# Optimization experiments

Hardware: AMD Instinct MI355X
Metric: run time of the kernel (lower is better)

The kernel has to match this reference:

```python
import jax, jax.numpy as jnp
import numpy as np
import math


def l2norm(x, axis):
    n = jnp.linalg.norm(x, axis=axis, keepdims=True)
    return x / jnp.maximum(n, 1e-12)


def token_pooling(x, w1, b1, w2, b2, p, w3, b3, w4, b4, eps=1e-6):
    # x: [B, L, dim_in]
    h = jnp.maximum(x @ w1 + b1, 0.0) @ w2 + b2        # [B, L, 512]
    h = l2norm(h, -1)
    # GeM over token dim L (avg_pool1d over full length == mean)
    g = jnp.mean(jnp.clip(h, eps, None) ** p, axis=1) ** (1.0 / p)  # [B, 512]
    o = jnp.maximum(g @ w3 + b3, 0.0) @ w4 + b4        # [B, dim_out]
    return l2norm(o, -1)


def sinkhorn_log(S_aug, log_a, log_b, num_iters=3):
    # S_aug: [B, m+1, n]; reg = 1.0
    M = S_aug
    u = jnp.zeros_like(log_a)
    v = jnp.zeros_like(log_b)
    def body(carry, _):
        u, v = carry
        u = log_a - jax.nn.logsumexp(M + v[:, None, :], axis=2)
        v = log_b - jax.nn.logsumexp(M + u[:, :, None], axis=1)
        return (u, v), None
    (u, v), _ = jax.lax.scan(body, (u, v), None, length=num_iters)
    return M + u[:, :, None] + v[:, None, :]


def setup_inputs() -> dict:
    key = jax.random.key(0)
    ks = jax.random.split(key, 16)
    B, S, N, C = 4, 4, 1029, 2048
    def w(k, shape):
        return jax.random.normal(k, shape, dtype=jnp.float32) * 0.02
    inp = {
        "tokens": jax.random.normal(ks[0], (B, S, N, C), dtype=jnp.float32),
        "patch_start_idx": 5,
        # camera token pooling
        "cam_w1": w(ks[1], (2048, 1024)), "cam_b1": jnp.zeros((1024,), jnp.float32),
        "cam_w2": w(ks[2], (1024, 512)),  "cam_b2": jnp.zeros((512,), jnp.float32),
        "cam_p":  jnp.ones((1,), jnp.float32) * 3.0,
        "cam_w3": w(ks[3], (512, 512)),   "cam_b3": jnp.zeros((512,), jnp.float32),
        "cam_w4": w(ks[4], (512, 256)),   "cam_b4": jnp.zeros((256,), jnp.float32),
        # register token pooling
        "reg_w1": w(ks[5], (2048, 1024)), "reg_b1": jnp.zeros((1024,), jnp.float32),
        "reg_w2": w(ks[6], (1024, 512)),  "reg_b2": jnp.zeros((512,), jnp.float32),
        "reg_p":  jnp.ones((1,), jnp.float32) * 3.0,
        "reg_w3": w(ks[7], (512, 512)),   "reg_b3": jnp.zeros((512,), jnp.float32),
        "reg_w4": w(ks[8], (512, 256)),   "reg_b4": jnp.zeros((256,), jnp.float32),
        # patch cluster features (1x1 convs == linear over channel dim)
        "pf_w1": w(ks[9], (2048, 512)),   "pf_b1": jnp.zeros((512,), jnp.float32),
        "pf_w2": w(ks[10], (512, 128)),   "pf_b2": jnp.zeros((128,), jnp.float32),
        # patch scores
        "ps_w1": w(ks[11], (2048, 512)),  "ps_b1": jnp.zeros((512,), jnp.float32),
        "ps_w2": w(ks[12], (512, 64)),    "ps_b2": jnp.zeros((64,), jnp.float32),
        "dust_bin": jnp.array(1.0, jnp.float32),
    }
    return inp


def reference(tokens, patch_start_idx, cam_w1, cam_b1, cam_w2, cam_b2, cam_p, cam_w3, cam_b3, cam_w4, cam_b4, reg_w1, reg_b1, reg_w2, reg_b2, reg_p, reg_w3, reg_b3, reg_w4, reg_b4, pf_w1, pf_b1, pf_w2, pf_b2, ps_w1, ps_b1, ps_w2, ps_b2, dust_bin):
    B, S, N, C = tokens.shape
    psi = int(patch_start_idx)
    # camera token: [B, S, C]
    camera = token_pooling(tokens[:, :, 0], cam_w1, cam_b1, cam_w2, cam_b2, cam_p, cam_w3, cam_b3, cam_w4, cam_b4)
    # register tokens: [B, S*(psi-1), C]
    reg_tok = tokens[:, :, 1:psi].reshape(B, S * (psi - 1), C)
    register = token_pooling(reg_tok, reg_w1, reg_b1, reg_w2, reg_b2, reg_p, reg_w3, reg_b3, reg_w4, reg_b4)
    # patch tokens flattened over (S, Np): n = S*Np
    patch = tokens[:, :, psi:].reshape(B, -1, C)              # [B, n, C]
    n = patch.shape[1]
    feats = jnp.maximum(patch @ pf_w1 + pf_b1, 0.0) @ pf_w2 + pf_b2   # [B, n, 128]
    scores = jnp.maximum(patch @ ps_w1 + ps_b1, 0.0) @ ps_w2 + ps_b2  # [B, n, 64]
    S_mat = jnp.swapaxes(scores, 1, 2)                        # [B, m, n]
    m = S_mat.shape[1]
    # augment with dustbin row
    dust_row = jnp.broadcast_to(dust_bin, (B, 1, n)).astype(S_mat.dtype)
    S_aug = jnp.concatenate([S_mat, dust_row], axis=1)        # [B, m+1, n]
    norm = -math.log(n + m)
    log_a = jnp.full((m + 1,), norm, dtype=S_mat.dtype).at[-1].add(math.log(n - m))
    log_b = jnp.full((n,), norm, dtype=S_mat.dtype)
    log_a = jnp.broadcast_to(log_a, (B, m + 1))
    log_b = jnp.broadcast_to(log_b, (B, n))
    log_P = sinkhorn_log(S_aug, log_a, log_b, num_iters=3) - norm
    p = jnp.exp(log_P)[:, :-1, :]                             # [B, m, n]
    # (f * p).sum(-1) as batched matmul: [B, cluster_dim, m]
    pooled = jnp.einsum('bnc,bkn->bck', feats, p)
    patch_result = l2norm(pooled, 1).reshape(B, -1)           # [B, cluster_dim*m]
    return jnp.concatenate([patch_result, camera, register], axis=-1)
```

## Files before the change

kernel.cpp:

```cpp
#include <hip/hip_runtime.h>

typedef unsigned short u16;
typedef unsigned int u32;

#define B_ 4
#define S_ 4
#define NTOK 1029
#define CDIM 2048
#define PSI 5
#define NPB 4096
#define MROWS 16384
#define N1 1024
#define N2 256
#define MD 64
#define MA 65

using bf16x8 = __attribute__((ext_vector_type(8))) short;
using f32x4  = __attribute__((ext_vector_type(4))) float;
using u16x8  = __attribute__((ext_vector_type(8))) unsigned short;

typedef __attribute__((address_space(1))) const void global_cvoid;
typedef __attribute__((address_space(3))) void lds_void;

__device__ __forceinline__ u16 f2b(float f) {
  u32 u = __builtin_bit_cast(u32, f);
  u32 r = (u + 0x7fffu + ((u >> 16) & 1u)) >> 16;
  return (u16)r;
}

__global__ void k_prep_patch(const float* __restrict__ tokens, u16* __restrict__ Abf,
                             const float* __restrict__ pfw1, const float* __restrict__ psw1,
                             const float* __restrict__ pfw2, const float* __restrict__ psw2,
                             const float* __restrict__ pfb1, const float* __restrict__ psb1,
                             const float* __restrict__ pfb2, const float* __restrict__ psb2,
                             u16* __restrict__ W1t, u16* __restrict__ W2t,
                             float* __restrict__ b1c, float* __restrict__ b2c) {
  __shared__ float tile[32][33];
  int id = blockIdx.x, tid = threadIdx.x;
  if (id < 16384) {
    size_t idx = (size_t)id * 256 + tid;
    size_t r = idx >> 8;
    int cv = (int)(idx & 255) << 3;
    int b = (int)(r >> 12), s = (int)((r >> 10) & 3), j = (int)(r & 1023);
    const float* src = tokens + ((size_t)((b * S_ + s) * NTOK + PSI + j)) * CDIM + cv;
    float4 v0 = *(const float4*)src;
    float4 v1 = *(const float4*)(src + 4);
    u16x8 o;
    o[0] = f2b(v0.x); o[1] = f2b(v0.y); o[2] = f2b(v0.z); o[3] = f2b(v0.w);
    o[4] = f2b(v1.x); o[5] = f2b(v1.y); o[6] = f2b(v1.z); o[7] = f2b(v1.w);
    *(u16x8*)(Abf + r * CDIM + cv) = o;
    return;
  }
  int id2 = id - 16384;
  int tx = tid & 31, ty = tid >> 5;
  if (id2 < 2048) {
    int kb = (id2 & 63) * 32, nb = (id2 >> 6) * 32;
    #pragma unroll
    for (int i = 0; i < 4; ++i) {
      int k = kb + ty + i * 8, n = nb + tx;
      tile[ty + i * 8][tx] = (n < 512) ? pfw1[(size_t)k * 512 + n] : psw1[(size_t)k * 512 + (n - 512)];
    }
    __syncthreads();
    #pragma unroll
    for (int i = 0; i < 4; ++i) {
      int n = nb + ty + i * 8, k = kb + tx;
      W1t[(size_t)n * CDIM + k] = f2b(tile[tx][ty + i * 8]);
    }
  } else if (id2 < 2304) {
    int i2 = id2 - 2048;
    int kb = (i2 & 31) * 32, jb = (i2 >> 5) * 32;
    #pragma unroll
    for (int i = 0; i < 4; ++i) {
      int k = kb + ty + i * 8, j = jb + tx;
      float v = 0.f;
      if (j < 128) { if (k < 512) v = pfw2[(size_t)k * 128 + j]; }
      else if (j < 192) { if (k >= 512) v = psw2[(size_t)(k - 512) * 64 + (j - 128)]; }
      tile[ty + i * 8][tx] = v;
    }
    __syncthreads();
    #pragma unroll
    for (int i = 0; i < 4; ++i) {
      int j = jb + ty + i * 8, k = kb + tx;
      W2t[(size_t)j * N1 + k] = f2b(tile[tx][ty + i * 8]);
    }
  } else {
    int t = (id2 - 2304) * 256 + tid;
    if (t < 1024) b1c[t] = (t < 512) ? pfb1[t] : psb1[t - 512];
    if (t < 256)  b2c[t] = (t < 128) ? pfb2[t] : ((t < 192) ? psb2[t - 128] : 0.f);
  }
}

__global__ void k_pack_cr(const float* __restrict__ camw1, const float* __restrict__ regw1,
                          const float* __restrict__ camw2, const float* __restrict__ regw2,
                          const float* __restrict__ tokens,
                          u16* __restrict__ Bt1cr, u16* __restrict__ Bt2cr,
                          u16* __restrict__ Acr) {
  __shared__ float tile[32][33];
  int id = blockIdx.x, tid = threadIdx.x;
  int tx = tid & 31, ty = tid >> 5;
  if (id < 4096) {
    const float* src = (id < 2048) ? camw1 : regw1;
    u16* dst = Bt1cr + ((id < 2048) ? 0 : (size_t)1024 * CDIM);
    int i2 = id & 2047;
    int kb = (i2 & 63) * 32, nb = (i2 >> 6) * 32;
    #pragma unroll
    for (int i = 0; i < 4; ++i)
      tile[ty + i * 8][tx] = src[(size_t)(kb + ty + i * 8) * 1024 + nb + tx];
    __syncthreads();
    #pragma unroll
    for (int i = 0; i < 4; ++i)
      dst[(size_t)(nb + ty + i * 8) * CDIM + kb + tx] = f2b(tile[tx][ty + i * 8]);
  } else if (id < 5120) {
    int i3 = id - 4096;
    const float* src = (i3 < 512) ? camw2 : regw2;
    u16* dst = Bt2cr + ((i3 < 512) ? 0 : (size_t)512 * N1);
    int i2 = i3 & 511;
    int kb = (i2 & 31) * 32, nb = (i2 >> 5) * 32;
    #pragma unroll
    for (int i = 0; i < 4; ++i)
      tile[ty + i * 8][tx] = src[(size_t)(kb + ty + i * 8) * 512 + nb + tx];
    __syncthreads();
    #pragma unroll
    for (int i = 0; i < 4; ++i)
      dst[(size_t)(nb + ty + i * 8) * N1 + kb + tx] = f2b(tile[tx][ty + i * 8]);
  } else {
    int r = id - 5120;
    int c0 = tid << 3;
    u16x8 o;
    if (r >= 80) {
      #pragma unroll
      for (int i = 0; i < 8; ++i) o[i] = 0;
    } else {
      const float* src;
      if (r < 16) { int b = r >> 2, s = r & 3; src = tokens + ((size_t)(b * S_ + s) * NTOK) * CDIM; }
      else { int r2 = r - 16; int b = r2 >> 4, q = r2 & 15, s = q >> 2, t = (q & 3) + 1;
             src = tokens + ((size_t)(b * S_ + s) * NTOK + t) * CDIM; }
      float4 v0 = *(const float4*)(src + c0);
      float4 v1 = *(const float4*)(src + c0 + 4);
      o[0] = f2b(v0.x); o[1] = f2b(v0.y); o[2] = f2b(v0.z); o[3] = f2b(v0.w);
      o[4] = f2b(v1.x); o[5] = f2b(v1.y); o[6] = f2b(v1.z); o[7] = f2b(v1.w);
    }
    *(u16x8*)(Acr + (size_t)r * CDIM + c0) = o;
  }
}

#define STAGE_TILE(buf, k0)                                                    \
  {                                                                            \
    _Pragma("unroll")                                                          \
    for (int r = 0; r < 4; ++r) {                                              \
      __builtin_amdgcn_global_load_lds(                                        \
          (global_cvoid*)(A + abase + (size_t)(r * 32) * K + (k0)),            \
          (lds_void*)(&As[buf][lofs + r * 2048]), 16, 0, 0);                   \
      __builtin_amdgcn_global_load_lds(                                        \
          (global_cvoid*)(Bt + bbase + (size_t)(r * 32) * K + (k0)),           \
          (lds_void*)(&Bs[buf][lofs + r * 2048]), 16, 0, 0);                   \
    }                                                                          \
  }

#define COMPUTE_TILE(buf)                                                      \
  {                                                                            \
    _Pragma("unroll")                                                          \
    for (int kk = 0; kk < 64; kk += 32) {                                      \
      const int csw = (kk + hi8) ^ ((lane & 7) << 3);                          \
      bf16x8 af[4], bfr[4];                                                    \
      _Pragma("unroll")                                                        \
      for (int i = 0; i < 4; ++i) {                                            \
        af[i]  = *(const bf16x8*)&As[buf][((wr << 6) + (i << 4) + (lane & 15)) * 64 + csw]; \
        bfr[i] = *(const bf16x8*)&Bs[buf][((wc << 6) + (i << 4) + (lane & 15)) * 64 + csw]; \
      }                                                                        \
      _Pragma("unroll")                                                        \
      for (int mi = 0; mi < 4; ++mi)                                           \
        _Pragma("unroll")                                                      \
        for (int ni = 0; ni < 4; ++ni)                                         \
          acc[mi][ni] = __builtin_amdgcn_mfma_f32_16x16x32_bf16(af[mi], bfr[ni], acc[mi][ni], 0, 0, 0); \
    }                                                                          \
  }

template <int RELU, int OUTBF, int WRSC>
__global__ __launch_bounds__(256, 2)
void k_gemm(const u16* __restrict__ A, const u16* __restrict__ Bt,
            const float* __restrict__ bias, void* __restrict__ Cout,
            int M, int N, int K, float* __restrict__ ScOut) {
  __shared__ u16 As[2][128 * 64];
  __shared__ u16 Bs[2][128 * 64];
  const int tid = threadIdx.x;
  const int lane = tid & 63;
  const int wave = tid >> 6;
  const int tM = blockIdx.x << 7;
  const int tN = blockIdx.y << 7;
  const int wr = wave >> 1, wc = wave & 1;
  const int hi8 = (lane >> 4) << 3;

  const int srow = (wave << 3) + (lane >> 3);
  const int scolsw = ((lane & 7) ^ (lane >> 3)) << 3;
  const size_t abase = (size_t)(tM + srow) * K + scolsw;
  const size_t bbase = (size_t)(tN + srow) * K + scolsw;
  const int lofs = (wave << 9) + (lane << 3);

  f32x4 acc[4][4];
  #pragma unroll
  for (int i = 0; i < 4; ++i)
    #pragma unroll
    for (int j = 0; j < 4; ++j)
      acc[i][j] = (f32x4){0.f, 0.f, 0.f, 0.f};

  const int nt = K >> 6;
  STAGE_TILE(0, 0)
  STAGE_TILE(1, 64)
  for (int t = 0; t < nt; t += 2) {
    asm volatile("s_waitcnt vmcnt(8)" ::: "memory");
    __builtin_amdgcn_s_barrier();
    COMPUTE_TILE(0)
    __builtin_amdgcn_s_barrier();
    if (t + 2 < nt) STAGE_TILE(0, (t + 2) << 6)
    if (t + 1 == nt - 1) {
      asm volatile("s_waitcnt vmcnt(0)" ::: "memory");
    } else {
      asm volatile("s_waitcnt vmcnt(8)" ::: "memory");
    }
    __builtin_amdgcn_s_barrier();
    COMPUTE_TILE(1)
    __builtin_amdgcn_s_barrier();
    if (t + 3 < nt) STAGE_TILE(1, (t + 3) << 6)
  }

  #pragma unroll
  for (int ni = 0; ni < 4; ++ni) {
    const int col = tN + (wc << 6) + (ni << 4) + (lane & 15);
    const float bv = bias[col];
    #pragma unroll
    for (int mi = 0; mi < 4; ++mi) {
      #pragma unroll
      for (int j = 0; j < 4; ++j) {
        const int row = tM + (wr << 6) + (mi << 4) + ((lane >> 4) << 2) + j;
        float vv = acc[mi][ni][j] + bv;
        if (RELU) vv = fmaxf(vv, 0.f);
        if (OUTBF) ((u16*)Cout)[(size_t)row * N + col] = f2b(vv);
        else       ((float*)Cout)[(size_t)row * N + col] = vv;
        if (WRSC) {
          if (col >= 128 && col < 192)
            ScOut[((size_t)((row >> 12) * MD + (col - 128))) * NPB + (row & 4095)] = vv;
        }
      }
    }
  }
}

__global__ __launch_bounds__(256, 2)
void k_gemm_splitk(const u16* __restrict__ A, const u16* __restrict__ Bt,
                   float* __restrict__ part, int N, int K, int KC) {
  __shared__ u16 As1[128 * 64];
  __shared__ u16 Bs1[128 * 64];
  const int tid = threadIdx.x;
  const int lane = tid & 63;
  const int wave = tid >> 6;
  const int tN = blockIdx.y << 7;
  const int kb = blockIdx.z * KC;
  const int wr = wave >> 1, wc = wave & 1;
  const int srow = (wave << 3) + (lane >> 3);
  const int scol = (lane & 7) << 3;
  const size_t abase = (size_t)srow * K + scol;
  const size_t bbase = (size_t)(tN + srow) * K + scol;
  u16* asw = &As1[(wave << 9) + (lane << 3)];
  u16* bsw = &Bs1[(wave << 9) + (lane << 3)];

  f32x4 acc[4][4];
  #pragma unroll
  for (int i = 0; i < 4; ++i)
    #pragma unroll
    for (int j = 0; j < 4; ++j)
      acc[i][j] = (f32x4){0.f, 0.f, 0.f, 0.f};

  for (int k0 = kb; k0 < kb + KC; k0 += 64) {
    #pragma unroll
    for (int r = 0; r < 4; ++r) {
      __builtin_amdgcn_global_load_lds(
          (global_cvoid*)(A + abase + (size_t)(r * 32) * K + k0),
          (lds_void*)(asw + r * 2048), 16, 0, 0);
      __builtin_amdgcn_global_load_lds(
          (global_cvoid*)(Bt + bbase + (size_t)(r * 32) * K + k0),
          (lds_void*)(bsw + r * 2048), 16, 0, 0);
    }
    __syncthreads();
    #pragma unroll
    for (int kk = 0; kk < 64; kk += 32) {
      bf16x8 af[4], bfr[4];
      #pragma unroll
      for (int i = 0; i < 4; ++i) {
        af[i]  = *(const bf16x8*)&As1[((wr << 6) + (i << 4) + (lane & 15)) * 64 + kk + ((lane >> 4) << 3)];
        bfr[i] = *(const bf16x8*)&Bs1[((wc << 6) + (i << 4) + (lane & 15)) * 64 + kk + ((lane >> 4) << 3)];
      }
      #pragma unroll
      for (int mi = 0; mi < 4; ++mi)
        #pragma unroll
        for (int ni = 0; ni < 4; ++ni)
          acc[mi][ni] = __builtin_amdgcn_mfma_f32_16x16x32_bf16(af[mi], bfr[ni], acc[mi][ni], 0, 0, 0);
    }
    __syncthreads();
  }

  float* dst = part + (size_t)blockIdx.z * 128 * N;
  #pragma unroll
  for (int ni = 0; ni < 4; ++ni) {
    const int col = tN + (wc << 6) + (ni << 4) + (lane & 15);
    #pragma unroll
    for (int mi = 0; mi < 4; ++mi) {
      #pragma unroll
      for (int j = 0; j < 4; ++j) {
        const int row = (wr << 6) + (mi << 4) + ((lane >> 4) << 2) + j;
        dst[(size_t)row * N + col] = acc[mi][ni][j];
      }
    }
  }
}

__global__ void k_cr_fin1(const float* __restrict__ part1,
                          const float* __restrict__ camb1, const float* __restrict__ regb1,
                          u16* __restrict__ A2) {
  int r = blockIdx.x;
  int j = blockIdx.y * 256 + threadIdx.x;
  if (r >= 80) { A2[(size_t)r * N1 + j] = 0; return; }
  bool cam = (r < 16);
  int cm = j + (cam ? 0 : 1024);
  float s = 0.f;
  #pragma unroll
  for (int kc = 0; kc < 8; ++kc) s += part1[((size_t)kc * 128 + r) * 2048 + cm];
  s += cam ? camb1[j] : regb1[j];
  A2[(size_t)r * N1 + j] = f2b(fmaxf(s, 0.f));
}

__global__ __launch_bounds__(512)
void k_cr_fin2(const float* __restrict__ part2,
               const float* __restrict__ camb2, const float* __restrict__ regb2,
               const float* __restrict__ camp, const float* __restrict__ regp,
               float* __restrict__ hp) {
  __shared__ float red[8];
  int r = blockIdx.x;
  int j = threadIdx.x;
  bool cam = (r < 16);
  int cm = j + (cam ? 0 : 512);
  float s = 0.f;
  #pragma unroll
  for (int kc = 0; kc < 8; ++kc) s += part2[((size_t)kc * 128 + r) * 1024 + cm];
  s += cam ? camb2[j] : regb2[j];
  float ss = s * s;
  #pragma unroll
  for (int o = 32; o; o >>= 1) ss += __shfl_down(ss, o);
  if ((j & 63) == 0) red[j >> 6] = ss;
  __syncthreads();
  float tot = 0.f;
  #pragma unroll
  for (int i = 0; i < 8; ++i) tot += red[i];
  float inv = 1.f / fmaxf(sqrtf(tot), 1e-12f);
  float t = fmaxf(s * inv, 1e-6f);
  hp[(size_t)r * 512 + j] = powf(t, cam ? camp[0] : regp[0]);
}

__global__ __launch_bounds__(512)
void k_cr3a(const float* __restrict__ hp, const float* __restrict__ camp,
            const float* __restrict__ regp, float* __restrict__ gsb) {
  int pb = blockIdx.x;
  bool cam = (pb < 4);
  int b = pb & 3;
  float p = cam ? camp[0] : regp[0];
  int L = cam ? 4 : 16;
  int row0 = cam ? b * 4 : 16 + b * 16;
  int o = threadIdx.x;
  float s = 0.f;
  for (int r = 0; r < L; ++r) s += hp[(size_t)(row0 + r) * 512 + o];
  gsb[pb * 512 + o] = powf(s / (float)L, 1.f / p);
}

__global__ __launch_bounds__(512)
void k_cr3b(const float* __restrict__ gsb,
            const float* __restrict__ camw3, const float* __restrict__ regw3,
            const float* __restrict__ camb3, const float* __restrict__ regb3,
            float* __restrict__ o1b) {
  __shared__ float gls[512];
  __shared__ float part[4][128];
  int pb = blockIdx.x, och = blockIdx.y;
  bool cam = (pb < 4);
  const float* W3 = cam ? camw3 : regw3;
  const float* B3 = cam ? camb3 : regb3;
  int tid = threadIdx.x;
  gls[tid] = gsb[pb * 512 + tid];
  __syncthreads();
  int col = tid & 127, kq = tid >> 7;
  int o = (och << 7) + col;
  float acc = 0.f;
  const float* w = W3 + (size_t)(kq << 7) * 512 + o;
  #pragma unroll 8
  for (int kk = 0; kk < 128; ++kk) acc += gls[(kq << 7) + kk] * w[(size_t)kk * 512];
  part[kq][col] = acc;
  __syncthreads();
  if (kq == 0) {
    float s = part[0][col] + part[1][col] + part[2][col] + part[3][col] + B3[o];
    o1b[pb * 512 + o] = fmaxf(s, 0.f);
  }
}

__global__ __launch_bounds__(512)
void k_cr3c(const float* __restrict__ o1b,
            const float* __restrict__ camw4, const float* __restrict__ regw4,
            const float* __restrict__ camb4, const float* __restrict__ regb4,
            float* __restrict__ out) {
  __shared__ float o1s[512];
  __shared__ float part[2][256];
  __shared__ float vsq[256];
  __shared__ float red[4];
  int pb = blockIdx.x;
  bool cam = (pb < 4);
  int path = pb >> 2, b = pb & 3;
  const float* W4 = cam ? camw4 : regw4;
  const float* B4 = cam ? camb4 : regb4;
  int tid = threadIdx.x;
  o1s[tid] = o1b[pb * 512 + tid];
  __syncthreads();
  int col = tid & 255, kh = tid >> 8;
  float acc = 0.f;
  const float* w = W4 + (size_t)(kh << 8) * 256 + col;
  #pragma unroll 8
  for (int kk = 0; kk < 256; ++kk) acc += o1s[(kh << 8) + kk] * w[(size_t)kk * 256];
  part[kh][col] = acc;
  __syncthreads();
  float val = 0.f;
  if (kh == 0) {
    val = part[0][col] + part[1][col] + B4[col];
    vsq[col] = val * val;
  }
  __syncthreads();
  float ss = (tid < 256) ? vsq[tid] : 0.f;
  #pragma unroll
  for (int o = 32; o; o >>= 1) ss += __shfl_down(ss, o);
  if (tid < 256 && (tid & 63) == 0) red[tid >> 6] = ss;
  __syncthreads();
  if (kh == 0) {
    float tot = red[0] + red[1] + red[2] + red[3];
    float inv = 1.f / fmaxf(sqrtf(tot), 1e-12f);
    out[(size_t)b * 8704 + 8192 + path * 256 + col] = val * inv;
  }
}

__global__ void k_sink_u(const float* __restrict__ Sc, const float* __restrict__ v,
                         float* __restrict__ u, const float* __restrict__ dust) {
  __shared__ float redm[4], reds[4];
  int b = blockIdx.x / MA, k = blockIdx.x % MA;
  const float* vb = v + (size_t)b * NPB;
  int tid = threadIdx.x;
  float mx = -1e30f, s = 0.f;
  if (k < MD) {
    const float* row = Sc + ((size_t)(b * MD) + k) * NPB;
    for (int n = tid; n < NPB; n += 256) {
      float x = row[n] + vb[n];
      float m2 = fmaxf(mx, x);
      s = s * __expf(mx - m2) + __expf(x - m2);
      mx = m2;
    }
  } else {
    float d0 = dust[0];
    for (int n = tid; n < NPB; n += 256) {
      float x = d0 + vb[n];
      float m2 = fmaxf(mx, x);
      s = s * __expf(mx - m2) + __expf(x - m2);
      mx = m2;
    }
  }
  #pragma unroll
  for (int o = 32; o; o >>= 1) {
    float mo = __shfl_down(mx, o), so = __shfl_down(s, o);
    float m2 = fmaxf(mx, mo);
    s = s * __expf(mx - m2) + so * __expf(mo - m2);
    mx = m2;
  }
  if ((tid & 63) == 0) { redm[tid >> 6] = mx; reds[tid >> 6] = s; }
  __syncthreads();
  if (tid == 0) {
    float M = redm[0];
    #pragma unroll
    for (int i = 1; i < 4; ++i) M = fmaxf(M, redm[i]);
    float S = 0.f;
    #pragma unroll
    for (int i = 0; i < 4; ++i) S += reds[i] * __expf(redm[i] - M);
    const float nrm = -logf((float)(NPB + MD));
    float la = (k == MD) ? (nrm + logf((float)(NPB - MD))) : nrm;
    u[b * MA + k] = la - (M + __logf(S));
  }
}

__global__ void k_sink_v(const float* __restrict__ Sc, const float* __restrict__ u,
                         float* __restrict__ v, const float* __restrict__ dust) {
  __shared__ float us[MA];
  int b = blockIdx.x >> 4;
  int n = ((blockIdx.x & 15) << 8) + threadIdx.x;
  if (threadIdx.x < MA) us[threadIdx.x] = u[b * MA + threadIdx.x];
  __syncthreads();
  const float* Sb = Sc + (size_t)b * MD * NPB + n;
  float d0 = dust[0];
  float mx = d0 + us[MD];
  for (int k = 0; k < MD; ++k) mx = fmaxf(mx, Sb[(size_t)k * NPB] + us[k]);
  float s = __expf(d0 + us[MD] - mx);
  for (int k = 0; k < MD; ++k) s += __expf(Sb[(size_t)k * NPB] + us[k] - mx);
  const float nrm = -logf((float)(NPB + MD));
  v[(size_t)b * NPB + n] = nrm - (mx + __logf(s));
}

__global__ __launch_bounds__(256)
void k_pooled1(const float* __restrict__ FS, const float* __restrict__ Sc,
               const float* __restrict__ u, const float* __restrict__ v,
               float* __restrict__ partial) {
  __shared__ float Fs[64][132];
  __shared__ float Ps[64][68];
  int b = blockIdx.x >> 6, j = blockIdx.x & 63;
  int n0 = j << 6;
  int tid = threadIdx.x;
  {
    int r = tid >> 5;
    int c4 = (tid & 31) << 2;
    #pragma unroll
    for (int i = 0; i < 8; ++i) {
      int n = r + (i << 3);
      float4 vv = *(const float4*)&FS[((size_t)(b * NPB + n0 + n)) * N2 + c4];
      *(float4*)&Fs[n][c4] = vv;
    }
  }
  {
    const float nrm = -logf((float)(NPB + MD));
    int r = tid >> 4;
    int c4 = (tid & 15) << 2;
    #pragma unroll
    for (int i = 0; i < 4; ++i) {
      int k = r + (i << 4);
      float uk = u[b * MA + k];
      float4 sv = *(const float4*)&Sc[((size_t)(b * MD) + k) * NPB + n0 + c4];
      float4 vv = *(const float4*)&v[(size_t)b * NPB + n0 + c4];
      float4 o;
      o.x = __expf(sv.x + uk + vv.x - nrm);
      o.y = __expf(sv.y + uk + vv.y - nrm);
      o.z = __expf(sv.z + uk + vv.z - nrm);
      o.w = __expf(sv.w + uk + vv.w - nrm);
      *(float4*)&Ps[k][c4] = o;
    }
  }
  __syncthreads();
  int tc = tid & 31, tk = tid >> 5;
  int c0 = tc << 2, k0 = tk << 3;
  float acc[4][8];
  #pragma unroll
  for (int i = 0; i < 4; ++i)
    #pragma unroll
    for (int kk = 0; kk < 8; ++kk) acc[i][kk] = 0.f;
  for (int n = 0; n < 64; ++n) {
    float4 f = *(const float4*)&Fs[n][c0];
    float pv[8];
    #pragma unroll
    for (int kk = 0; kk < 8; ++kk) pv[kk] = Ps[k0 + kk][n];
    #pragma unroll
    for (int i = 0; i < 4; ++i) {
      float fv = ((const float*)&f)[i];
      #pragma unroll
      for (int kk = 0; kk < 8; ++kk) acc[i][kk] += fv * pv[kk];
    }
  }
  float* dst = partial + ((size_t)(b * 64 + j) << 13);
  #pragma unroll
  for (int i = 0; i < 4; ++i) {
    float4 lo = {acc[i][0], acc[i][1], acc[i][2], acc[i][3]};
    float4 hi = {acc[i][4], acc[i][5], acc[i][6], acc[i][7]};
    *(float4*)&dst[((c0 + i) << 6) + k0] = lo;
    *(float4*)&dst[((c0 + i) << 6) + k0 + 4] = hi;
  }
}

__global__ void k_pooled2(const float* __restrict__ partial, float* __restrict__ pooled) {
  int o = blockIdx.x * 256 + threadIdx.x;
  int b = o >> 13, rem = o & 8191;
  const float* src = partial + ((size_t)b << 19) + rem;
  float s = 0.f;
  #pragma unroll 8
  for (int j = 0; j < 64; ++j) s += src[(size_t)j << 13];
  pooled[o] = s;
}

__global__ void k_patch_out(const float* __restrict__ pooled, float* __restrict__ out) {
  int b = blockIdx.x >> 6, k = blockIdx.x & 63;
  int tid = threadIdx.x;
  float v0 = pooled[((size_t)(b * 128) + tid) * MD + k];
  float v1 = pooled[((size_t)(b * 128) + 64 + tid) * MD + k];
  float ss = v0 * v0 + v1 * v1;
  #pragma unroll
  for (int o = 32; o; o >>= 1) ss += __shfl_down(ss, o);
  ss = __shfl(ss, 0);
  float inv = 1.f / fmaxf(sqrtf(ss), 1e-12f);
  out[(size_t)b * 8704 + tid * 64 + k] = v0 * inv;
  out[(size_t)b * 8704 + (64 + tid) * 64 + k] = v1 * inv;
}

#define OFF_ABF 0u
#define OFF_SC 0u
#define OFF_U 4259840u
#define OFF_V 4263936u
#define OFF_POOL 8523776u
#define OFF_HP 8982528u
#define OFF_H 67108864u
#define OFF_PART OFF_H
#define OFF_CP1 75497472u
#define OFF_GSB OFF_CP1
#define OFF_O1B 75513856u
#define OFF_CP2 83886080u
#define OFF_BT1CR 88080384u
#define OFF_BT2CR 96468992u
#define OFF_ACR 98566144u
#define OFF_A2 99090432u
#define OFF_FS 100663296u
#define OFF_W1T 117440512u
#define OFF_W2T 121634816u
#define OFF_B1C 122159104u
#define OFF_B2C 122163200u

extern "C" void kernel_launch(void* const* d_in, const int* in_sizes, int n_in,
                              void* d_out, int out_size, void* d_ws, size_t ws_size,
                              hipStream_t stream) {
  (void)in_sizes; (void)n_in; (void)out_size; (void)ws_size;
  const float* tokens = (const float*)d_in[0];
  const float* cam_w1 = (const float*)d_in[2];
  const float* cam_b1 = (const float*)d_in[3];
  const float* cam_w2 = (const float*)d_in[4];
  const float* cam_b2 = (const float*)d_in[5];
  const float* cam_p  = (const float*)d_in[6];
  const float* cam_w3 = (const float*)d_in[7];
  const float* cam_b3 = (const float*)d_in[8];
  const float* cam_w4 = (const float*)d_in[9];
  const float* cam_b4 = (const float*)d_in[10];
  const float* reg_w1 = (const float*)d_in[11];
  const float* reg_b1 = (const float*)d_in[12];
  const float* reg_w2 = (const float*)d_in[13];
  const float* reg_b2 = (const float*)d_in[14];
  const float* reg_p  = (const float*)d_in[15];
  const float* reg_w3 = (const float*)d_in[16];
  const float* reg_b3 = (const float*)d_in[17];
  const float* reg_w4 = (const float*)d_in[18];
  const float* reg_b4 = (const float*)d_in[19];
  const float* pf_w1  = (const float*)d_in[20];
  const float* pf_b1  = (const float*)d_in[21];
  const float* pf_w2  = (const float*)d_in[22];
  const float* pf_b2  = (const float*)d_in[23];
  const float* ps_w1  = (const float*)d_in[24];
  const float* ps_b1  = (const float*)d_in[25];
  const float* ps_w2  = (const float*)d_in[26];
  const float* ps_b2  = (const float*)d_in[27];
  const float* dust   = (const float*)d_in[28];
  float* out = (float*)d_out;
  char* ws = (char*)d_ws;

  u16* Abf = (u16*)(ws + OFF_ABF);
  float* Sc = (float*)(ws + OFF_SC);
  float* ub = (float*)(ws + OFF_U);
  float* vb = (float*)(ws + OFF_V);
  float* pooled = (float*)(ws + OFF_POOL);
  float* hp = (float*)(ws + OFF_HP);
  u16* H   = (u16*)(ws + OFF_H);
  float* partial = (float*)(ws + OFF_PART);
  float* cp1 = (float*)(ws + OFF_CP1);
  float* gsb = (float*)(ws + OFF_GSB);
  float* o1b = (float*)(ws + OFF_O1B);
  float* cp2 = (float*)(ws + OFF_CP2);
  u16* Bt1cr = (u16*)(ws + OFF_BT1CR);
  u16* Bt2cr = (u16*)(ws + OFF_BT2CR);
  u16* Acr = (u16*)(ws + OFF_ACR);
  u16* A2  = (u16*)(ws + OFF_A2);
  float* FS = (float*)(ws + OFF_FS);
  u16* W1t = (u16*)(ws + OFF_W1T);
  u16* W2t = (u16*)(ws + OFF_W2T);
  float* b1c = (float*)(ws + OFF_B1C);
  float* b2c = (float*)(ws + OFF_B2C);

  hipMemsetAsync(vb, 0, (size_t)B_ * NPB * sizeof(float), stream);

  k_prep_patch<<<18692, 256, 0, stream>>>(tokens, Abf, pf_w1, ps_w1, pf_w2, ps_w2,
                                          pf_b1, ps_b1, pf_b2, ps_b2,
                                          W1t, W2t, b1c, b2c);
  k_gemm<1, 1, 0><<<dim3(128, 8), 256, 0, stream>>>(Abf, W1t, b1c, (void*)H,
                                                    MROWS, N1, CDIM, nullptr);
  k_gemm<0, 0, 1><<<dim3(128, 2), 256, 0, stream>>>(H, W2t, b2c, (void*)FS,
                                                    MROWS, N2, N1, Sc);

  k_pack_cr<<<5248, 256, 0, stream>>>(cam_w1, reg_w1, cam_w2, reg_w2, tokens,
                                      Bt1cr, Bt2cr, Acr);
  k_gemm_splitk<<<dim3(1, 16, 8), 256, 0, stream>>>(Acr, Bt1cr, cp1, 2048, CDIM, 256);
  k_cr_fin1<<<dim3(128, 4), 256, 0, stream>>>(cp1, cam_b1, reg_b1, A2);
  k_gemm_splitk<<<dim3(1, 8, 8), 256, 0, stream>>>(A2, Bt2cr, cp2, 1024, N1, 128);
  k_cr_fin2<<<80, 512, 0, stream>>>(cp2, cam_b2, reg_b2, cam_p, reg_p, hp);
  k_cr3a<<<8, 512, 0, stream>>>(hp, cam_p, reg_p, gsb);
  k_cr3b<<<dim3(8, 4), 512, 0, stream>>>(gsb, cam_w3, reg_w3, cam_b3, reg_b3, o1b);
  k_cr3c<<<8, 512, 0, stream>>>(o1b, cam_w4, reg_w4, cam_b4, reg_b4, out);

  for (int it = 0; it < 3; ++it) {
    k_sink_u<<<B_ * MA, 256, 0, stream>>>(Sc, vb, ub, dust);
    k_sink_v<<<B_ * 16, 256, 0, stream>>>(Sc, ub, vb, dust);
  }
  k_pooled1<<<B_ * 64, 256, 0, stream>>>(FS, Sc, ub, vb, partial);
  k_pooled2<<<128, 256, 0, stream>>>(partial, pooled);
  k_patch_out<<<B_ * MD, 64, 0, stream>>>(pooled, out);
}
```

Before: 243.1 us.

## Fuse camera/register head kernels and restructure Sinkhorn column update

Merges the three small pooling-head kernels (GeM mean, first MLP layer, second MLP layer with L2 norm) into one kernel per batch/path, so two launches and the global round-trips through scratch buffers are gone. The fused kernel uses 8 blocks, so the first MLP layer, which was previously spread over 32 blocks, now runs over output chunks serially inside each block. Separately, the Sinkhorn v-update now uses 256 blocks of 64 threads instead of 64 blocks of 256, stages the score tile in shared memory, and computes the logsumexp with an online single pass instead of two passes.

```diff
diff --git a/kernel.cpp b/kernel.cpp
--- a/kernel.cpp
+++ b/kernel.cpp
@@ -357,75 +357,67 @@
 }
 
 __global__ __launch_bounds__(512)
-void k_cr3a(const float* __restrict__ hp, const float* __restrict__ camp,
-            const float* __restrict__ regp, float* __restrict__ gsb) {
-  int pb = blockIdx.x;
-  bool cam = (pb < 4);
-  int b = pb & 3;
-  float p = cam ? camp[0] : regp[0];
-  int L = cam ? 4 : 16;
-  int row0 = cam ? b * 4 : 16 + b * 16;
-  int o = threadIdx.x;
-  float s = 0.f;
-  for (int r = 0; r < L; ++r) s += hp[(size_t)(row0 + r) * 512 + o];
-  gsb[pb * 512 + o] = powf(s / (float)L, 1.f / p);
-}
-
-__global__ __launch_bounds__(512)
-void k_cr3b(const float* __restrict__ gsb,
-            const float* __restrict__ camw3, const float* __restrict__ regw3,
-            const float* __restrict__ camb3, const float* __restrict__ regb3,
-            float* __restrict__ o1b) {
+void k_cr3f(const float* __restrict__ hp,
+            const float* __restrict__ camp, const float* __restrict__ camw3,
+            const float* __restrict__ camb3, const float* __restrict__ camw4,
+            const float* __restrict__ camb4,
+            const float* __restrict__ regp, const float* __restrict__ regw3,
+            const float* __restrict__ regb3, const float* __restrict__ regw4,
+            const float* __restrict__ regb4,
+            float* __restrict__ out) {
   __shared__ float gls[512];
-  __shared__ float part[4][128];
-  int pb = blockIdx.x, och = blockIdx.y;
-  bool cam = (pb < 4);
-  const float* W3 = cam ? camw3 : regw3;
-  const float* B3 = cam ? camb3 : regb3;
-  int tid = threadIdx.x;
-  gls[tid] = gsb[pb * 512 + tid];
-  __syncthreads();
-  int col = tid & 127, kq = tid >> 7;
-  int o = (och << 7) + col;
-  float acc = 0.f;
-  const float* w = W3 + (size_t)(kq << 7) * 512 + o;
-  #pragma unroll 8
-  for (int kk = 0; kk < 128; ++kk) acc += gls[(kq << 7) + kk] * w[(size_t)kk * 512];
-  part[kq][col] = acc;
-  __syncthreads();
-  if (kq == 0) {
-    float s = part[0][col] + part[1][col] + part[2][col] + part[3][col] + B3[o];
-    o1b[pb * 512 + o] = fmaxf(s, 0.f);
-  }
-}
-
-__global__ __launch_bounds__(512)
-void k_cr3c(const float* __restrict__ o1b,
-            const float* __restrict__ camw4, const float* __restrict__ regw4,
-            const float* __restrict__ camb4, const float* __restrict__ regb4,
-            float* __restrict__ out) {
   __shared__ float o1s[512];
-  __shared__ float part[2][256];
+  __shared__ float partb[4][128];
+  __shared__ float partc[2][256];
   __shared__ float vsq[256];
   __shared__ float red[4];
   int pb = blockIdx.x;
   bool cam = (pb < 4);
   int path = pb >> 2, b = pb & 3;
+  const float* W3 = cam ? camw3 : regw3;
+  const float* B3 = cam ? camb3 : regb3;
   const float* W4 = cam ? camw4 : regw4;
   const float* B4 = cam ? camb4 : regb4;
+  float p = cam ? camp[0] : regp[0];
+  int L = cam ? 4 : 16;
+  int row0 = cam ? b * 4 : 16 + b * 16;
   int tid = threadIdx.x;
-  o1s[tid] = o1b[pb * 512 + tid];
+
+  {
+    float s = 0.f;
+    for (int r = 0; r < L; ++r) s += hp[(size_t)(row0 + r) * 512 + tid];
+    gls[tid] = powf(s / (float)L, 1.f / p);
+  }
   __syncthreads();
+
+  {
+    int col = tid & 127, kq = tid >> 7;
+    for (int och = 0; och < 4; ++och) {
+      int oc = (och << 7) + col;
+      float acc = 0.f;
+      const float* w = W3 + (size_t)(kq << 7) * 512 + oc;
+      #pragma unroll 8
+      for (int kk = 0; kk < 128; ++kk) acc += gls[(kq << 7) + kk] * w[(size_t)kk * 512];
+      partb[kq][col] = acc;
+      __syncthreads();
+      if (kq == 0)
+        o1s[oc] = fmaxf(partb[0][col] + partb[1][col] + partb[2][col] + partb[3][col] + B3[oc], 0.f);
+      __syncthreads();
+    }
+  }
+
   int col = tid & 255, kh = tid >> 8;
   float acc = 0.f;
-  const float* w = W4 + (size_t)(kh << 8) * 256 + col;
-  #pragma unroll 8
-  for (int kk = 0; kk < 256; ++kk) acc += o1s[(kh << 8) + kk] * w[(size_t)kk * 256];
-  part[kh][col] = acc;
+  {
+    const float* w = W4 + (size_t)(kh << 8) * 256 + col;
+    #pragma unroll 8
+    for (int kk = 0; kk < 256; ++kk) acc += o1s[(kh << 8) + kk] * w[(size_t)kk * 256];
+    partc[kh][col] = acc;
+  }
   __syncthreads();
   float val = 0.f;
   if (kh == 0) {
-    val = part[0][col] + part[1][col] + B4[col];
+    val = partc[0][col] + partc[1][col] + B4[col];
     vsq[col] = val * val;
   }
   __syncthreads();
@@ -487,21 +479,31 @@
   }
 }
 
-__global__ void k_sink_v(const float* __restrict__ Sc, const float* __restrict__ u,
-                         float* __restrict__ v, const float* __restrict__ dust) {
+__global__ __launch_bounds__(64)
+void k_sink_v(const float* __restrict__ Sc, const float* __restrict__ u,
+              float* __restrict__ v, const float* __restrict__ dust) {
+  __shared__ float tile[64][65];
   __shared__ float us[MA];
-  int b = blockIdx.x >> 4;
-  int n = ((blockIdx.x & 15) << 8) + threadIdx.x;
-  if (threadIdx.x < MA) us[threadIdx.x] = u[b * MA + threadIdx.x];
+  int b = blockIdx.x >> 6;
+  int n0 = (blockIdx.x & 63) << 6;
+  int tid = threadIdx.x;
+  us[tid] = u[b * MA + tid];
+  if (tid == 0) us[MD] = u[b * MA + MD];
+  const float* Sb = Sc + (size_t)b * MD * NPB + n0;
+  #pragma unroll 8
+  for (int k = 0; k < MD; ++k)
+    tile[k][tid] = Sb[(size_t)k * NPB + tid];
   __syncthreads();
-  const float* Sb = Sc + (size_t)b * MD * NPB + n;
-  float d0 = dust[0];
-  float mx = d0 + us[MD];
-  for (int k = 0; k < MD; ++k) mx = fmaxf(mx, Sb[(size_t)k * NPB] + us[k]);
-  float s = __expf(d0 + us[MD] - mx);
-  for (int k = 0; k < MD; ++k) s += __expf(Sb[(size_t)k * NPB] + us[k] - mx);
+  float mx = dust[0] + us[MD], s = 1.f;
+  #pragma unroll 8
+  for (int k = 0; k < MD; ++k) {
+    float x = tile[k][tid] + us[k];
+    float m2 = fmaxf(mx, x);
+    s = s * __expf(mx - m2) + __expf(x - m2);
+    mx = m2;
+  }
   const float nrm = -logf((float)(NPB + MD));
-  v[(size_t)b * NPB + n] = nrm - (mx + __logf(s));
+  v[(size_t)b * NPB + n0 + tid] = nrm - (mx + __logf(s));
 }
 
 __global__ __launch_bounds__(256)
@@ -604,8 +606,6 @@
 #define OFF_H 67108864u
 #define OFF_PART OFF_H
 #define OFF_CP1 75497472u
-#define OFF_GSB OFF_CP1
-#define OFF_O1B 75513856u
 #define OFF_CP2 83886080u
 #define OFF_BT1CR 88080384u
 #define OFF_BT2CR 96468992u
@@ -661,8 +661,6 @@
   u16* H   = (u16*)(ws + OFF_H);
   float* partial = (float*)(ws + OFF_PART);
   float* cp1 = (float*)(ws + OFF_CP1);
-  float* gsb = (float*)(ws + OFF_GSB);
-  float* o1b = (float*)(ws + OFF_O1B);
   float* cp2 = (float*)(ws + OFF_CP2);
   u16* Bt1cr = (u16*)(ws + OFF_BT1CR);
   u16* Bt2cr = (u16*)(ws + OFF_BT2CR);
@@ -690,13 +688,12 @@
   k_cr_fin1<<<dim3(128, 4), 256, 0, stream>>>(cp1, cam_b1, reg_b1, A2);
   k_gemm_splitk<<<dim3(1, 8, 8), 256, 0, stream>>>(A2, Bt2cr, cp2, 1024, N1, 128);
   k_cr_fin2<<<80, 512, 0, stream>>>(cp2, cam_b2, reg_b2, cam_p, reg_p, hp);
-  k_cr3a<<<8, 512, 0, stream>>>(hp, cam_p, reg_p, gsb);
-  k_cr3b<<<dim3(8, 4), 512, 0, stream>>>(gsb, cam_w3, reg_w3, cam_b3, reg_b3, o1b);
-  k_cr3c<<<8, 512, 0, stream>>>(o1b, cam_w4, reg_w4, cam_b4, reg_b4, out);
+  k_cr3f<<<8, 512, 0, stream>>>(hp, cam_p, cam_w3, cam_b3, cam_w4, cam_b4,
+                                reg_p, reg_w3, reg_b3, reg_w4, reg_b4, out);
 
   for (int it = 0; it < 3; ++it) {
     k_sink_u<<<B_ * MA, 256, 0, stream>>>(Sc, vb, ub, dust);
-    k_sink_v<<<B_ * 16, 256, 0, stream>>>(Sc, ub, vb, dust);
+    k_sink_v<<<B_ * 64, 64, 0, stream>>>(Sc, ub, vb, dust);
   }
   k_pooled1<<<B_ * 64, 256, 0, stream>>>(FS, Sc, ub, vb, partial);
   k_pooled2<<<128, 256, 0, stream>>>(partial, pooled);
```

New measurement: 258.9 us. 1.06x slower.
